# Kernel tuning notes

Measured on AMD Instinct MI355X. Metric: run time of the kernel, lower is better.

## Reference

```python
import jax, jax.numpy as jnp
import numpy as np

L = 4          # num_layers
D = 64         # embedding_dim
N = 100000     # nodes
E = 1250000    # edges
B = 2048       # graphs (batch.max()+1, fixed for jit)
ATOM_V = 128   # atom feature vocab per field
BOND_V = 8     # bond feature vocab per field
BN_EPS = 1e-5


def setup_inputs() -> dict:
    key = jax.random.key(0)
    ks = jax.random.split(key, 10)
    x_feat = jax.random.randint(ks[0], (N, 9), 0, 119)
    edge_index = jax.random.randint(ks[1], (2, E), 0, N)
    edge_attr = jax.random.randint(ks[2], (E, 3), 0, 5)
    batch = jnp.sort(jax.random.randint(ks[3], (N,), 0, B))
    s = 0.02
    atom_emb = jax.random.normal(ks[4], (9, ATOM_V, D), jnp.float32) * s
    bond_emb = jax.random.normal(ks[5], (L, 3, BOND_V, D), jnp.float32) * s
    eps = jnp.zeros((L,), jnp.float32)
    W1 = jax.random.normal(ks[6], (L, D, 2 * D), jnp.float32) / np.sqrt(D).astype(np.float32)
    b1 = jnp.zeros((L, 2 * D), jnp.float32)
    bn1_g = jnp.ones((L, 2 * D), jnp.float32)
    bn1_b = jnp.zeros((L, 2 * D), jnp.float32)
    W2 = jax.random.normal(ks[7], (L, 2 * D, D), jnp.float32) / np.sqrt(2 * D).astype(np.float32)
    b2 = jnp.zeros((L, D), jnp.float32)
    bn2_g = jnp.ones((L, D), jnp.float32)
    bn2_b = jnp.zeros((L, D), jnp.float32)
    return dict(atom_emb=atom_emb, bond_emb=bond_emb, eps=eps,
                W1=W1, b1=b1, bn1_g=bn1_g, bn1_b=bn1_b,
                W2=W2, b2=b2, bn2_g=bn2_g, bn2_b=bn2_b,
                x_feat=x_feat, edge_index=edge_index, edge_attr=edge_attr, batch=batch)


def _bn(h, g, b):
    # training-mode BatchNorm1d over node dim (biased variance, as torch forward)
    m = h.mean(axis=0)
    v = jnp.mean((h - m) ** 2, axis=0)
    return (h - m) * jax.lax.rsqrt(v + BN_EPS) * g + b


def reference(atom_emb, bond_emb, eps, W1, b1, bn1_g, bn1_b, W2, b2, bn2_g, bn2_b,
              x_feat, edge_index, edge_attr, batch):
    n = x_feat.shape[0]
    # AtomEncoder: sum of per-field embedding lookups -> [N, D]
    h = atom_emb[jnp.arange(9), x_feat].sum(axis=1)
    src, dst = edge_index[0], edge_index[1]
    for l in range(L):
        # BondEncoder for this layer: [E, D]
        e = bond_emb[l][jnp.arange(3), edge_attr].sum(axis=1)
        # message: relu(x_j + edge_emb); aggregate: scatter_add at target nodes
        msg = jax.nn.relu(h[src] + e)
        agg = jax.ops.segment_sum(msg, dst, num_segments=N)
        z = (1.0 + eps[l]) * h + agg
        # MLP: Linear -> BN -> ReLU -> Linear
        z = jax.nn.relu(_bn(z @ W1[l] + b1[l], bn1_g[l], bn1_b[l]))
        z = z @ W2[l] + b2[l]
        # outer per-layer BatchNorm
        h = _bn(z, bn2_g[l], bn2_b[l])
        if l != L - 1:
            h = jax.nn.relu(h)
        # dropout disabled (eval/deterministic reference)
    node_repr = h
    # mean pooling by graph id
    out_feat = jax.ops.segment_sum(h, batch, num_segments=B)
    cnt = jax.ops.segment_sum(jnp.ones((n, 1), h.dtype), batch, num_segments=B)
    graph_repr = out_feat / (cnt + 1e-9)
    return node_repr, graph_repr
```

## Files before the change

### kernel.cpp

```cpp
#include <hip/hip_runtime.h>

#define NN 100000
#define NE 1250000
#define NB 2048
#define NZB 391
#define NBK 196
#define BCAP 7168
#define ARND 2048

typedef __attribute__((ext_vector_type(8))) short short8;
typedef __attribute__((ext_vector_type(4))) float floatx4;

__device__ inline unsigned short f2bf(float f) {
    unsigned u = __float_as_uint(f);
    u = u + 0x7fffu + ((u >> 16) & 1u);
    return (unsigned short)(u >> 16);
}
__device__ inline float bf2f(unsigned short h) {
    return __uint_as_float(((unsigned)h) << 16);
}

__global__ void atom_encode(const float* __restrict__ atom_emb,
                            const int* __restrict__ x_feat,
                            float* __restrict__ h, unsigned short* __restrict__ h16) {
    int id = blockIdx.x * 256 + threadIdx.x;
    int n = id >> 4, q = id & 15;
    floatx4 acc = {0.f, 0.f, 0.f, 0.f};
    for (int f = 0; f < 9; f++) {
        int v = x_feat[n * 9 + f];
        const floatx4* p = (const floatx4*)(atom_emb + (size_t)(f * 128 + v) * 64);
        acc += p[q];
    }
    ((floatx4*)h)[(size_t)n * 16 + q] = acc;
    ushort4 hv;
    hv.x = f2bf(acc[0]); hv.y = f2bf(acc[1]); hv.z = f2bf(acc[2]); hv.w = f2bf(acc[3]);
    ((ushort4*)h16)[(size_t)n * 16 + q] = hv;
}


__launch_bounds__(256)
__global__ void bucketA(const int* __restrict__ ei, const int* __restrict__ ea,
                        int* __restrict__ bcnt, unsigned long long* __restrict__ bbuf) {
    __shared__ int cnt[256], inc[256], cur[256], gpos[256];
    __shared__ unsigned long long buf[ARND];
    __shared__ unsigned short bos[ARND];
    int tid = threadIdx.x;
    cnt[tid] = 0; cur[tid] = 0;
    __syncthreads();
    int base = blockIdx.x * ARND;
    unsigned long long rec[8]; int bb[8];
    #pragma unroll
    for (int i = 0; i < 8; i++) {
        int e = base + i * 256 + tid;
        if (e < NE) {
            int src = ei[e];
            int dst = ei[NE + e];
            unsigned at = (unsigned)(ea[e * 3] | (ea[e * 3 + 1] << 3) | (ea[e * 3 + 2] << 6));
            rec[i] = ((unsigned long long)(unsigned)dst << 32)
                   | (unsigned)src | (at << 17);
            bb[i] = dst >> 9;
            atomicAdd(&cnt[bb[i]], 1);
        } else bb[i] = -1;
    }
    __syncthreads();
    int v = cnt[tid];
    inc[tid] = v;
    __syncthreads();
    for (int d = 1; d < 256; d <<= 1) {
        int t = (tid >= d) ? inc[tid - d] : 0;
        __syncthreads();
        inc[tid] += t;
        __syncthreads();
    }
    if (v > 0) gpos[tid] = atomicAdd(&bcnt[tid], v);
    __syncthreads();
    #pragma unroll
    for (int i = 0; i < 8; i++) {
        if (bb[i] >= 0) {
            int b = bb[i];
            int p = atomicAdd(&cur[b], 1);
            int slot = (inc[b] - cnt[b]) + p;
            buf[slot] = rec[i];
            bos[slot] = (unsigned short)b;
        }
    }
    __syncthreads();
    int nval = inc[255];
    for (int s = tid; s < nval; s += 256) {
        int b = bos[s];
        int off = s - (inc[b] - cnt[b]);
        bbuf[(size_t)b * BCAP + gpos[b] + off] = buf[s];
    }
}

__launch_bounds__(256)
__global__ void bucketB(const int* __restrict__ bcnt,
                        const unsigned long long* __restrict__ bbuf,
                        int* __restrict__ csr, unsigned* __restrict__ epack) {
    __shared__ int c[512], cs[512], s[256], bp[256], sh[1];
    __shared__ unsigned long long fl[BCAP];
    int tid = threadIdx.x;
    int b = blockIdx.x;
    bp[tid] = (tid < NBK) ? bcnt[tid] : 0;
    c[tid] = 0; c[256 + tid] = 0;
    __syncthreads();
    for (int d = 1; d < 256; d <<= 1) {
        int t = (tid >= d) ? bp[tid - d] : 0;
        __syncthreads();
        bp[tid] += t;
        __syncthreads();
    }
    int gbase = b ? bp[b - 1] : 0;
    int cnt = bcnt[b];
    const unsigned long long* f = bbuf + (size_t)b * BCAP;
    int n0 = b << 9;
    for (int i = tid; i < cnt; i += 256) {
        unsigned long long v = f[i];
        fl[i] = v;
        atomicAdd(&c[(int)(v >> 32) - n0], 1);
    }
    __syncthreads();
    cs[tid] = c[tid]; cs[256 + tid] = c[256 + tid];
    s[tid] = c[tid];
    __syncthreads();
    for (int d = 1; d < 256; d <<= 1) {
        int t = (tid >= d) ? s[tid - d] : 0;
        __syncthreads();
        s[tid] += t;
        __syncthreads();
    }
    c[tid] = s[tid];
    if (tid == 255) sh[0] = s[255];
    __syncthreads();
    s[tid] = c[256 + tid];
    __syncthreads();
    for (int d = 1; d < 256; d <<= 1) {
        int t = (tid >= d) ? s[tid - d] : 0;
        __syncthreads();
        s[tid] += t;
        __syncthreads();
    }
    c[256 + tid] = s[tid] + sh[0];
    __syncthreads();
    int nn = NN - n0; if (nn > 512) nn = 512;
    for (int i = tid; i < 512; i += 256) {
        int start = gbase + c[i] - cs[i];
        if (i < nn) csr[n0 + i] = gbase + c[i];
        cs[i] = start;
    }
    __syncthreads();
    for (int t = 0; t < 8; t++) {
        for (int i = tid; i < cnt; i += 256) {
            unsigned long long v = fl[i];
            if ((int)((v & 0x1FFFFu) >> 14) == t) {
                int idx = (int)(v >> 32) - n0;
                int p = atomicAdd(&cs[idx], 1);
                epack[p] = (unsigned)v;
            }
        }
        __syncthreads();
    }
}

#define PROC(hh, rr, A)                                                       \
    {                                                                         \
        floatx4 m = {bf2f(hh.x), bf2f(hh.y), bf2f(hh.z), bf2f(hh.w)};         \
        if (HASBN) {                                                          \
            m[0] = fmaxf(cav[0] * m[0] + cbv[0], 0.f);                        \
            m[1] = fmaxf(cav[1] * m[1] + cbv[1], 0.f);                        \
            m[2] = fmaxf(cav[2] * m[2] + cbv[2], 0.f);                        \
            m[3] = fmaxf(cav[3] * m[3] + cbv[3], 0.f);                        \
        }                                                                     \
        m += beq[((rr >> 17) & 7u) * 16 + q];                                 \
        m += beq[(8 + ((rr >> 20) & 7u)) * 16 + q];                           \
        m += beq[(16 + ((rr >> 23) & 7u)) * 16 + q];                          \
        A[0] += fmaxf(m[0], 0.f);                                             \
        A[1] += fmaxf(m[1], 0.f);                                             \
        A[2] += fmaxf(m[2], 0.f);                                             \
        A[3] += fmaxf(m[3], 0.f);                                             \
    }

template <bool HASBN>
__global__ void gather_k(const float* __restrict__ x, const unsigned short* __restrict__ x16,
                         const float* __restrict__ bond_emb,
                         const float* __restrict__ eps, const int* __restrict__ csr,
                         const unsigned* __restrict__ epack, int l,
                         const float* __restrict__ stats, const float* __restrict__ bn_g,
                         const float* __restrict__ bn_b, float* __restrict__ agg) {
    __shared__ float be[24 * 64];
    __shared__ float ca[64], cb[64];
    int tid = threadIdx.x;
    const float* bsrc = bond_emb + (size_t)l * 1536;
    for (int i = tid; i < 1536; i += 256) be[i] = bsrc[i];
    if (tid < 64) {
        if (HASBN) {
            float s = 0.f, ss = 0.f;
            for (int j = 0; j < 8; j++) {
                s  += stats[j * 128 + tid];
                ss += stats[j * 128 + 64 + tid];
            }
            float mean = s / NN;
            float var  = ss / NN - mean * mean;
            float a = bn_g[(l - 1) * 64 + tid] * rsqrtf(var + 1e-5f);
            ca[tid] = a;
            cb[tid] = bn_b[(l - 1) * 64 + tid] - mean * a;
        } else {
            ca[tid] = 1.f; cb[tid] = 0.f;
        }
    }
    __syncthreads();
    int id = blockIdx.x * 256 + tid;
    int n = id >> 4, q = id & 15;
    float s = 1.0f + eps[l];
    floatx4 cav = *(const floatx4*)&ca[q * 4];
    floatx4 cbv = *(const floatx4*)&cb[q * 4];
    floatx4 xv = ((const floatx4*)x)[(size_t)n * 16 + q];
    if (HASBN) {
        xv[0] = fmaxf(cav[0] * xv[0] + cbv[0], 0.f);
        xv[1] = fmaxf(cav[1] * xv[1] + cbv[1], 0.f);
        xv[2] = fmaxf(cav[2] * xv[2] + cbv[2], 0.f);
        xv[3] = fmaxf(cav[3] * xv[3] + cbv[3], 0.f);
    }
    floatx4 acc = xv * s;
    floatx4 accB = {0.f, 0.f, 0.f, 0.f};
    int k0 = n ? csr[n - 1] : 0;
    int k1 = csr[n];
    const floatx4* beq = (const floatx4*)be;
    const ushort4* xq = (const ushort4*)x16;
    int k = k0;
    for (; k + 3 < k1; k += 4) {
        unsigned r0 = epack[k];
        unsigned r1 = epack[k + 1];
        unsigned r2 = epack[k + 2];
        unsigned r3 = epack[k + 3];
        ushort4 h0 = xq[(size_t)(r0 & 0x1FFFFu) * 16 + q];
        ushort4 h1 = xq[(size_t)(r1 & 0x1FFFFu) * 16 + q];
        ushort4 h2 = xq[(size_t)(r2 & 0x1FFFFu) * 16 + q];
        ushort4 h3 = xq[(size_t)(r3 & 0x1FFFFu) * 16 + q];
        __builtin_amdgcn_sched_barrier(0);
        PROC(h0, r0, acc)
        PROC(h1, r1, accB)
        PROC(h2, r2, acc)
        PROC(h3, r3, accB)
    }
    for (; k < k1; k++) {
        unsigned r0 = epack[k];
        ushort4 h0 = xq[(size_t)(r0 & 0x1FFFFu) * 16 + q];
        PROC(h0, r0, acc)
    }
    acc += accB;
    ((floatx4*)agg)[(size_t)n * 16 + q] = acc;
}

__global__ void wcvt(const float* __restrict__ W1, const float* __restrict__ W2,
                     unsigned short* __restrict__ w1h, unsigned short* __restrict__ w2h) {
    int id = blockIdx.x * 256 + threadIdx.x;
    if (id < 32768) {
        int l = id >> 13, rem = id & 8191, c = rem >> 6, k = rem & 63;
        w1h[id] = f2bf(W1[l * 8192 + k * 128 + c]);
    } else {
        int id2 = id - 32768;
        int l = id2 >> 13, rem = id2 & 8191, c = rem >> 7, k = rem & 127;
        w2h[id2] = f2bf(W2[l * 8192 + k * 64 + c]);
    }
}

#define MFMA __builtin_amdgcn_mfma_f32_16x16x32_bf16

#define ZS 264
__launch_bounds__(256)
__global__ void zstat(const float* __restrict__ z, float* __restrict__ G,
                      float* __restrict__ zsum) {
    __shared__ char smem[67584];
    unsigned short* zh = (unsigned short*)smem;
    unsigned short* zl = zh + 64 * ZS;
    int tid = threadIdx.x;
    int c2 = tid & 31;
    int nof = tid >> 5;
    int wv = tid >> 6, lane = tid & 63, m = lane & 15, qd = lane >> 4;
    float2 csum = make_float2(0.f, 0.f);
    floatx4 acc[8];
    for (int t = 0; t < 8; t++) acc[t] = (floatx4){0.f, 0.f, 0.f, 0.f};
    int base = blockIdx.x * 256;
    for (int it = 0; it < 32; it++) {
        int n = it * 8 + nof;
        int node = base + n;
        float2 v = make_float2(0.f, 0.f);
        if (node < NN) v = ((const float2*)z)[(size_t)node * 32 + c2];
        csum.x += v.x; csum.y += v.y;
        unsigned short hx = f2bf(v.x), hy = f2bf(v.y);
        zh[(2 * c2) * ZS + n] = hx;
        zh[(2 * c2 + 1) * ZS + n] = hy;
        zl[(2 * c2) * ZS + n] = f2bf(v.x - bf2f(hx));
        zl[(2 * c2 + 1) * ZS + n] = f2bf(v.y - bf2f(hy));
    }
    __syncthreads();
    for (int kc = 0; kc < 8; kc++) {
        short8 ah = *(const short8*)&zh[(wv * 16 + m) * ZS + kc * 32 + qd * 8];
        for (int j = 0; j < 4; j++) {
            short8 bh = *(const short8*)&zh[(j * 16 + m) * ZS + kc * 32 + qd * 8];
            short8 bl = *(const short8*)&zl[(j * 16 + m) * ZS + kc * 32 + qd * 8];
            acc[j * 2]     = MFMA(ah, bh, acc[j * 2], 0, 0, 0);
            acc[j * 2 + 1] = MFMA(ah, bl, acc[j * 2 + 1], 0, 0, 0);
        }
    }
    for (int j = 0; j < 4; j++)
        for (int r = 0; r < 4; r++) {
            int idx = (wv * 16 + qd * 4 + r) * 64 + j * 16 + m;
            atomicAdd(&G[idx], acc[j * 2][r]);
            atomicAdd(&G[4096 + idx], acc[j * 2 + 1][r]);
        }
    __syncthreads();
    float* red = (float*)smem;
    red[tid] = csum.x; red[256 + tid] = csum.y;
    __syncthreads();
    if (tid < 32) {
        float sx = 0.f, sy = 0.f;
        for (int k = 0; k < 8; k++) { sx += red[k * 32 + tid]; sy += red[256 + k * 32 + tid]; }
        atomicAdd(&zsum[2 * tid], sx);
        atomicAdd(&zsum[2 * tid + 1], sy);
    }
}

__launch_bounds__(256)
__global__ void bn1stat(const float* __restrict__ W1, const float* __restrict__ b1,
                        const float* __restrict__ G, const float* __restrict__ zsum,
                        int l, const float* __restrict__ bn_g, const float* __restrict__ bn_b,
                        float* __restrict__ cab) {
    __shared__ float wc[64];
    __shared__ float red[256];
    int c = blockIdx.x;
    int tid = threadIdx.x;
    if (tid < 64) wc[tid] = bf2f(f2bf(W1[l * 8192 + tid * 128 + c]));
    __syncthreads();
    float q = 0.f;
    for (int p = 0; p < 16; p++) {
        int idx = p * 256 + tid;
        int i = idx >> 6, j = idx & 63;
        q += wc[i] * wc[j] * (G[idx] + 2.f * G[4096 + idx]);
    }
    red[tid] = q;
    __syncthreads();
    for (int d = 128; d > 0; d >>= 1) {
        if (tid < d) red[tid] += red[tid + d];
        __syncthreads();
    }
    if (tid == 0) {
        float s1 = 0.f;
        for (int k = 0; k < 64; k++) s1 += zsum[k] * wc[k];
        float bc = b1[l * 128 + c];
        double mean = ((double)s1 + (double)NN * (double)bc) / (double)NN;
        double ex2  = ((double)red[0] + 2.0 * (double)bc * (double)s1
                       + (double)NN * (double)bc * (double)bc) / (double)NN;
        float var = (float)(ex2 - mean * mean);
        float a = bn_g[l * 128 + c] * rsqrtf(var + 1e-5f);
        cab[c] = a;
        cab[128 + c] = bn_b[l * 128 + c] - (float)mean * a + a * bc;
    }
}

#define RS 140
__launch_bounds__(256, 4)
__global__ void mlp_fused(const float* __restrict__ z,
                          const unsigned short* __restrict__ w1h,
                          const unsigned short* __restrict__ w2h,
                          const float* __restrict__ b2,
                          const float* __restrict__ cab, int l,
                          float* __restrict__ t2, unsigned short* __restrict__ t216,
                          float* __restrict__ s2f) {
    __shared__ unsigned short smem[4 * 2 * 16 * RS];
    int tid = threadIdx.x;
    int wv = tid >> 6, lane = tid & 63, m = lane & 15, qd = lane >> 4;
    int base = blockIdx.x * 64;
    unsigned short* rbh = smem + wv * (2 * 16 * RS);
    unsigned short* rbl = rbh + 16 * RS;

    int row = base + wv * 16 + m;
    floatx4 z0a = {0.f, 0.f, 0.f, 0.f}, z0b = z0a, z1a = z0a, z1b = z0a;
    if (row < NN) {
        const floatx4* zp = (const floatx4*)z + (size_t)row * 16;
        z0a = zp[qd * 2];
        z0b = zp[qd * 2 + 1];
        z1a = zp[8 + qd * 2];
        z1b = zp[8 + qd * 2 + 1];
    }
    short8 ah0, al0, ah1, al1;
    for (int j = 0; j < 4; j++) {
        unsigned short h;
        h = f2bf(z0a[j]); ah0[j] = (short)h; al0[j] = (short)f2bf(z0a[j] - bf2f(h));
        h = f2bf(z0b[j]); ah0[4 + j] = (short)h; al0[4 + j] = (short)f2bf(z0b[j] - bf2f(h));
        h = f2bf(z1a[j]); ah1[j] = (short)h; al1[j] = (short)f2bf(z1a[j] - bf2f(h));
        h = f2bf(z1b[j]); ah1[4 + j] = (short)h; al1[4 + j] = (short)f2bf(z1b[j] - bf2f(h));
    }

    float caT[8], cbT[8];
    #pragma unroll
    for (int t = 0; t < 8; t++) {
        caT[t] = cab[t * 16 + m];
        cbT[t] = cab[128 + t * 16 + m];
    }

    const unsigned short* w1p = w1h + l * 8192;
    floatx4 acc1[8];
    #pragma unroll
    for (int t = 0; t < 8; t++) {
        const unsigned short* wp = w1p + (t * 16 + m) * 64;
        short8 bh0 = *(const short8*)(wp + qd * 8);
        short8 bh1 = *(const short8*)(wp + 32 + qd * 8);
        floatx4 c0 = {0.f, 0.f, 0.f, 0.f};
        c0 = MFMA(ah0, bh0, c0, 0, 0, 0);
        c0 = MFMA(al0, bh0, c0, 0, 0, 0);
        c0 = MFMA(ah1, bh1, c0, 0, 0, 0);
        c0 = MFMA(al1, bh1, c0, 0, 0, 0);
        acc1[t] = c0;
    }

    #pragma unroll
    for (int t = 0; t < 8; t++) {
        float a = caT[t], b = cbT[t];
        #pragma unroll
        for (int r = 0; r < 4; r++) {
            int rl = qd * 4 + r;
            float rv = fmaxf(a * acc1[t][r] + b, 0.f);
            unsigned short hh = f2bf(rv);
            rbh[rl * RS + t * 16 + m] = hh;
            rbl[rl * RS + t * 16 + m] = f2bf(rv - bf2f(hh));
        }
    }
    short8 ahf[4], alf[4];
    #pragma unroll
    for (int kh = 0; kh < 4; kh++) {
        ahf[kh] = *(const short8*)&rbh[m * RS + kh * 32 + qd * 8];
        alf[kh] = *(const short8*)&rbl[m * RS + kh * 32 + qd * 8];
    }

    const unsigned short* w2p = w2h + l * 8192;
    floatx4 acc2[4];
    #pragma unroll
    for (int t = 0; t < 4; t++) {
        const unsigned short* wp = w2p + (t * 16 + m) * 128;
        floatx4 c0 = {0.f, 0.f, 0.f, 0.f};
        #pragma unroll
        for (int kh = 0; kh < 4; kh++) {
            short8 bh = *(const short8*)(wp + kh * 32 + qd * 8);
            c0 = MFMA(ahf[kh], bh, c0, 0, 0, 0);
            c0 = MFMA(alf[kh], bh, c0, 0, 0, 0);
        }
        acc2[t] = c0;
    }

    float* redw = (float*)rbh;
    const float* bias = b2 + l * 64;
    #pragma unroll
    for (int t = 0; t < 4; t++) {
        int col = t * 16 + m;
        float bv = bias[col];
        float s = 0.f, ss = 0.f;
        #pragma unroll
        for (int r = 0; r < 4; r++) {
            int node = base + wv * 16 + qd * 4 + r;
            if (node < NN) {
                float v = acc2[t][r] + bv;
                t2[(size_t)node * 64 + col] = v;
                t216[(size_t)node * 64 + col] = f2bf(v);
                s += v; ss += v * v;
            }
        }
        redw[col * 4 + qd] = s;
        redw[256 + col * 4 + qd] = ss;
    }
    __syncthreads();
    if (tid < 64) {
        float s = 0.f, ss = 0.f;
        for (int w = 0; w < 4; w++) {
            const float* rw = (const float*)(smem + w * (2 * 16 * RS));
            for (int q = 0; q < 4; q++) {
                s  += rw[tid * 4 + q];
                ss += rw[256 + tid * 4 + q];
            }
        }
        float* dst = s2f + (blockIdx.x & 7) * 128;
        atomicAdd(&dst[tid], s);
        atomicAdd(&dst[64 + tid], ss);
    }
}

__global__ void bnapply_last(const float* __restrict__ t2, const float* __restrict__ bn_g,
                             const float* __restrict__ bn_b, const float* __restrict__ s2f,
                             float* __restrict__ out, float* __restrict__ gsum,
                             float* __restrict__ gcnt, const int* __restrict__ batch) {
    __shared__ float ca[64], cb[64];
    int tid = threadIdx.x;
    if (tid < 64) {
        float s = 0.f, ss = 0.f;
        for (int j = 0; j < 8; j++) {
            s  += s2f[j * 128 + tid];
            ss += s2f[j * 128 + 64 + tid];
        }
        float mean = s / NN;
        float var  = ss / NN - mean * mean;
        float a = bn_g[3 * 64 + tid] * rsqrtf(var + 1e-5f);
        ca[tid] = a;
        cb[tid] = bn_b[3 * 64 + tid] - mean * a;
    }
    __syncthreads();
    int c = tid & 63, nsub = tid >> 6;
    int nodebase = blockIdx.x * 64;
    float accv = 0.f, accc = 0.f;
    int curg = -1;
    for (int it = 0; it < 16; it++) {
        int node = nodebase + it * 4 + nsub;
        if (node < NN) {
            float v = ca[c] * t2[(size_t)node * 64 + c] + cb[c];
            out[(size_t)node * 64 + c] = v;
            int g = batch[node];
            if (g != curg) {
                if (curg >= 0) {
                    atomicAdd(&gsum[(size_t)curg * 64 + c], accv);
                    if (c == 0) atomicAdd(&gcnt[curg], accc);
                }
                curg = g; accv = v; accc = 1.f;
            } else {
                accv += v; accc += 1.f;
            }
        }
    }
    if (curg >= 0) {
        atomicAdd(&gsum[(size_t)curg * 64 + c], accv);
        if (c == 0) atomicAdd(&gcnt[curg], accc);
    }
}

__global__ void pool_div(const float* __restrict__ gsum, const float* __restrict__ gcnt,
                         float* __restrict__ out) {
    int id = blockIdx.x * 256 + threadIdx.x;
    int g = id >> 6;
    out[(size_t)NN * 64 + id] = gsum[id] / (gcnt[g] + 1e-9f);
}

extern "C" void kernel_launch(void* const* d_in, const int* in_sizes, int n_in,
                              void* d_out, int out_size, void* d_ws, size_t ws_size,
                              hipStream_t stream) {
    const float* atom_emb = (const float*)d_in[0];
    const float* bond_emb = (const float*)d_in[1];
    const float* eps      = (const float*)d_in[2];
    const float* W1       = (const float*)d_in[3];
    const float* b1       = (const float*)d_in[4];
    const float* bn1_g    = (const float*)d_in[5];
    const float* bn1_b    = (const float*)d_in[6];
    const float* W2       = (const float*)d_in[7];
    const float* b2       = (const float*)d_in[8];
    const float* bn2_g    = (const float*)d_in[9];
    const float* bn2_b    = (const float*)d_in[10];
    const int* x_feat     = (const int*)d_in[11];
    const int* edge_index = (const int*)d_in[12];
    const int* edge_attr  = (const int*)d_in[13];
    const int* batch      = (const int*)d_in[14];
    float* out = (float*)d_out;

    char* ws = (char*)d_ws;
    float* gsum   = (float*)ws;   ws += (size_t)NB * 64 * 4;
    float* gcnt   = (float*)ws;   ws += NB * 4;
    float* zsum   = (float*)ws;   ws += 4 * 64 * 4;
    float* G      = (float*)ws;   ws += (size_t)4 * 8192 * 4;
    float* s2f    = (float*)ws;   ws += (size_t)4 * 8 * 128 * 4;
    int* bcnt     = (int*)ws;     ws += 256 * 4;
    size_t zbytes = (size_t)(ws - (char*)d_ws);
    int* csr        = (int*)ws;       ws += (size_t)NN * 4;
    float* cab      = (float*)ws;     ws += 256 * 4;
    unsigned* epack = (unsigned*)ws;  ws += (size_t)NE * 4;
    float* xbuf = (float*)ws;     ws += (size_t)NN * 64 * 4;
    unsigned short* x16 = (unsigned short*)ws; ws += (size_t)NN * 64 * 2;
    float* agg  = (float*)ws;     ws += (size_t)NN * 64 * 4;
    unsigned short* w1h = (unsigned short*)ws; ws += 32768 * 2;
    unsigned short* w2h = (unsigned short*)ws; ws += 32768 * 2;
    unsigned long long* bbuf = (unsigned long long*)ws; ws += (size_t)NBK * BCAP * 8;

    hipMemsetAsync((void*)gsum, 0, zbytes, stream);

    wcvt<<<256, 256, 0, stream>>>(W1, W2, w1h, w2h);
    bucketA<<<(NE + ARND - 1) / ARND, 256, 0, stream>>>(edge_index, edge_attr, bcnt, bbuf);
    bucketB<<<NBK, 256, 0, stream>>>(bcnt, bbuf, csr, epack);
    atom_encode<<<6250, 256, 0, stream>>>(atom_emb, x_feat, xbuf, x16);

    for (int l = 0; l < 4; l++) {
        if (l == 0) {
            gather_k<false><<<6250, 256, 0, stream>>>(xbuf, x16, bond_emb, eps, csr, epack, l,
                                                      nullptr, nullptr, nullptr, agg);
        } else {
            gather_k<true><<<6250, 256, 0, stream>>>(xbuf, x16, bond_emb, eps, csr, epack, l,
                                                     s2f + (size_t)(l - 1) * 1024,
                                                     bn2_g, bn2_b, agg);
        }
        float* Gl = G + (size_t)l * 8192;
        zstat<<<NZB, 256, 0, stream>>>(agg, Gl, zsum + l * 64);
        bn1stat<<<128, 256, 0, stream>>>(W1, b1, Gl, zsum + l * 64, l, bn1_g, bn1_b, cab);
        mlp_fused<<<1563, 256, 0, stream>>>(agg, w1h, w2h, b2, cab, l,
                                            xbuf, x16, s2f + (size_t)l * 1024);
    }
    bnapply_last<<<1563, 256, 0, stream>>>(xbuf, bn2_g, bn2_b, s2f + (size_t)3 * 1024,
                                           out, gsum, gcnt, batch);
    pool_div<<<512, 256, 0, stream>>>(gsum, gcnt, out);
}
```

Baseline: 740.2 us.

## Merge prep kernels into one launch and fold BN1 stats into zstat last block

```diff
diff --git a/kernel.cpp b/kernel.cpp
--- a/kernel.cpp
+++ b/kernel.cpp
@@ -7,6 +7,7 @@
 #define NBK 196
 #define BCAP 7168
 #define ARND 2048
+#define NAB 611
 
 typedef __attribute__((ext_vector_type(8))) short short8;
 typedef __attribute__((ext_vector_type(4))) float floatx4;
@@ -20,76 +21,88 @@
     return __uint_as_float(((unsigned)h) << 16);
 }
 
-__global__ void atom_encode(const float* __restrict__ atom_emb,
-                            const int* __restrict__ x_feat,
-                            float* __restrict__ h, unsigned short* __restrict__ h16) {
-    int id = blockIdx.x * 256 + threadIdx.x;
-    int n = id >> 4, q = id & 15;
-    floatx4 acc = {0.f, 0.f, 0.f, 0.f};
-    for (int f = 0; f < 9; f++) {
-        int v = x_feat[n * 9 + f];
-        const floatx4* p = (const floatx4*)(atom_emb + (size_t)(f * 128 + v) * 64);
-        acc += p[q];
-    }
-    ((floatx4*)h)[(size_t)n * 16 + q] = acc;
-    ushort4 hv;
-    hv.x = f2bf(acc[0]); hv.y = f2bf(acc[1]); hv.z = f2bf(acc[2]); hv.w = f2bf(acc[3]);
-    ((ushort4*)h16)[(size_t)n * 16 + q] = hv;
-}
-
-
 __launch_bounds__(256)
-__global__ void bucketA(const int* __restrict__ ei, const int* __restrict__ ea,
-                        int* __restrict__ bcnt, unsigned long long* __restrict__ bbuf) {
+__global__ void prep(const int* __restrict__ ei, const int* __restrict__ ea,
+                     int* __restrict__ bcnt, unsigned long long* __restrict__ bbuf,
+                     const float* __restrict__ atom_emb, const int* __restrict__ x_feat,
+                     float* __restrict__ h, unsigned short* __restrict__ h16,
+                     const float* __restrict__ W1, const float* __restrict__ W2,
+                     unsigned short* __restrict__ w1h, unsigned short* __restrict__ w2h) {
     __shared__ int cnt[256], inc[256], cur[256], gpos[256];
     __shared__ unsigned long long buf[ARND];
     __shared__ unsigned short bos[ARND];
     int tid = threadIdx.x;
-    cnt[tid] = 0; cur[tid] = 0;
-    __syncthreads();
-    int base = blockIdx.x * ARND;
-    unsigned long long rec[8]; int bb[8];
-    #pragma unroll
-    for (int i = 0; i < 8; i++) {
-        int e = base + i * 256 + tid;
-        if (e < NE) {
-            int src = ei[e];
-            int dst = ei[NE + e];
-            unsigned at = (unsigned)(ea[e * 3] | (ea[e * 3 + 1] << 3) | (ea[e * 3 + 2] << 6));
-            rec[i] = ((unsigned long long)(unsigned)dst << 32)
-                   | (unsigned)src | (at << 17);
-            bb[i] = dst >> 9;
-            atomicAdd(&cnt[bb[i]], 1);
-        } else bb[i] = -1;
-    }
-    __syncthreads();
-    int v = cnt[tid];
-    inc[tid] = v;
-    __syncthreads();
-    for (int d = 1; d < 256; d <<= 1) {
-        int t = (tid >= d) ? inc[tid - d] : 0;
-        __syncthreads();
-        inc[tid] += t;
-        __syncthreads();
-    }
-    if (v > 0) gpos[tid] = atomicAdd(&bcnt[tid], v);
-    __syncthreads();
-    #pragma unroll
-    for (int i = 0; i < 8; i++) {
-        if (bb[i] >= 0) {
-            int b = bb[i];
-            int p = atomicAdd(&cur[b], 1);
-            int slot = (inc[b] - cnt[b]) + p;
-            buf[slot] = rec[i];
-            bos[slot] = (unsigned short)b;
-        }
-    }
-    __syncthreads();
-    int nval = inc[255];
-    for (int s = tid; s < nval; s += 256) {
-        int b = bos[s];
-        int off = s - (inc[b] - cnt[b]);
-        bbuf[(size_t)b * BCAP + gpos[b] + off] = buf[s];
+    int bid = blockIdx.x;
+    if (bid < NAB) {
+        cnt[tid] = 0; cur[tid] = 0;
+        __syncthreads();
+        int base = bid * ARND;
+        unsigned long long rec[8]; int bb[8];
+        #pragma unroll
+        for (int i = 0; i < 8; i++) {
+            int e = base + i * 256 + tid;
+            if (e < NE) {
+                int src = ei[e];
+                int dst = ei[NE + e];
+                unsigned at = (unsigned)(ea[e * 3] | (ea[e * 3 + 1] << 3) | (ea[e * 3 + 2] << 6));
+                rec[i] = ((unsigned long long)(unsigned)dst << 32)
+                       | (unsigned)src | (at << 17);
+                bb[i] = dst >> 9;
+                atomicAdd(&cnt[bb[i]], 1);
+            } else bb[i] = -1;
+        }
+        __syncthreads();
+        int v = cnt[tid];
+        inc[tid] = v;
+        __syncthreads();
+        for (int d = 1; d < 256; d <<= 1) {
+            int t = (tid >= d) ? inc[tid - d] : 0;
+            __syncthreads();
+            inc[tid] += t;
+            __syncthreads();
+        }
+        if (v > 0) gpos[tid] = atomicAdd(&bcnt[tid], v);
+        __syncthreads();
+        #pragma unroll
+        for (int i = 0; i < 8; i++) {
+            if (bb[i] >= 0) {
+                int b = bb[i];
+                int p = atomicAdd(&cur[b], 1);
+                int slot = (inc[b] - cnt[b]) + p;
+                buf[slot] = rec[i];
+                bos[slot] = (unsigned short)b;
+            }
+        }
+        __syncthreads();
+        int nval = inc[255];
+        for (int s = tid; s < nval; s += 256) {
+            int b = bos[s];
+            int off = s - (inc[b] - cnt[b]);
+            bbuf[(size_t)b * BCAP + gpos[b] + off] = buf[s];
+        }
+    } else if (bid < NAB + 6250) {
+        int id = (bid - NAB) * 256 + tid;
+        int n = id >> 4, q = id & 15;
+        floatx4 acc = {0.f, 0.f, 0.f, 0.f};
+        for (int f = 0; f < 9; f++) {
+            int vv = x_feat[n * 9 + f];
+            const floatx4* p = (const floatx4*)(atom_emb + (size_t)(f * 128 + vv) * 64);
+            acc += p[q];
+        }
+        ((floatx4*)h)[(size_t)n * 16 + q] = acc;
+        ushort4 hv;
+        hv.x = f2bf(acc[0]); hv.y = f2bf(acc[1]); hv.z = f2bf(acc[2]); hv.w = f2bf(acc[3]);
+        ((ushort4*)h16)[(size_t)n * 16 + q] = hv;
+    } else {
+        int id = (bid - NAB - 6250) * 256 + tid;
+        if (id < 32768) {
+            int l = id >> 13, rem = id & 8191, c = rem >> 6, k = rem & 63;
+            w1h[id] = f2bf(W1[l * 8192 + k * 128 + c]);
+        } else {
+            int id2 = id - 32768;
+            int l = id2 >> 13, rem = id2 & 8191, c = rem >> 7, k = rem & 127;
+            w2h[id2] = f2bf(W2[l * 8192 + k * 64 + c]);
+        }
     }
 }
 
@@ -252,25 +265,15 @@
     ((floatx4*)agg)[(size_t)n * 16 + q] = acc;
 }
 
-__global__ void wcvt(const float* __restrict__ W1, const float* __restrict__ W2,
-                     unsigned short* __restrict__ w1h, unsigned short* __restrict__ w2h) {
-    int id = blockIdx.x * 256 + threadIdx.x;
-    if (id < 32768) {
-        int l = id >> 13, rem = id & 8191, c = rem >> 6, k = rem & 63;
-        w1h[id] = f2bf(W1[l * 8192 + k * 128 + c]);
-    } else {
-        int id2 = id - 32768;
-        int l = id2 >> 13, rem = id2 & 8191, c = rem >> 7, k = rem & 127;
-        w2h[id2] = f2bf(W2[l * 8192 + k * 64 + c]);
-    }
-}
-
 #define MFMA __builtin_amdgcn_mfma_f32_16x16x32_bf16
 
 #define ZS 264
 __launch_bounds__(256)
 __global__ void zstat(const float* __restrict__ z, float* __restrict__ G,
-                      float* __restrict__ zsum) {
+                      float* __restrict__ zsum,
+                      const float* __restrict__ W1, const float* __restrict__ b1,
+                      const float* __restrict__ bn_g, const float* __restrict__ bn_b,
+                      float* __restrict__ cab, int* __restrict__ zcnt, int l) {
     __shared__ char smem[67584];
     unsigned short* zh = (unsigned short*)smem;
     unsigned short* zl = zh + 64 * ZS;
@@ -320,37 +323,35 @@
         atomicAdd(&zsum[2 * tid], sx);
         atomicAdd(&zsum[2 * tid + 1], sy);
     }
-}
-
-__launch_bounds__(256)
-__global__ void bn1stat(const float* __restrict__ W1, const float* __restrict__ b1,
-                        const float* __restrict__ G, const float* __restrict__ zsum,
-                        int l, const float* __restrict__ bn_g, const float* __restrict__ bn_b,
-                        float* __restrict__ cab) {
-    __shared__ float wc[64];
-    __shared__ float red[256];
-    int c = blockIdx.x;
-    int tid = threadIdx.x;
-    if (tid < 64) wc[tid] = bf2f(f2bf(W1[l * 8192 + tid * 128 + c]));
-    __syncthreads();
-    float q = 0.f;
-    for (int p = 0; p < 16; p++) {
-        int idx = p * 256 + tid;
-        int i = idx >> 6, j = idx & 63;
-        q += wc[i] * wc[j] * (G[idx] + 2.f * G[4096 + idx]);
-    }
-    red[tid] = q;
-    __syncthreads();
-    for (int d = 128; d > 0; d >>= 1) {
-        if (tid < d) red[tid] += red[tid + d];
-        __syncthreads();
-    }
-    if (tid == 0) {
+    __threadfence();
+    int* flag = (int*)(smem + 2048);
+    if (tid == 0) flag[0] = atomicAdd(zcnt, 1);
+    __syncthreads();
+    if (flag[0] != NZB - 1) return;
+    __threadfence();
+    float* wcs = (float*)(smem + 4096);
+    const float* W1p = W1 + l * 8192;
+    for (int i2 = tid; i2 < 8192; i2 += 256) wcs[i2] = bf2f(f2bf(W1p[i2]));
+    __syncthreads();
+    int c = tid >> 1, hh = tid & 1;
+    const volatile float* Gv = G;
+    float qq = 0.f;
+    for (int i = hh * 32; i < hh * 32 + 32; i++) {
+        float wi = wcs[i * 128 + c];
+        for (int j = 0; j < 64; j++) {
+            float g0 = Gv[i * 64 + j];
+            float g1 = Gv[4096 + i * 64 + j];
+            qq += wi * wcs[j * 128 + c] * (g0 + 2.f * g1);
+        }
+    }
+    qq += __shfl_xor(qq, 1);
+    if (hh == 0) {
+        const volatile float* zs = zsum;
         float s1 = 0.f;
-        for (int k = 0; k < 64; k++) s1 += zsum[k] * wc[k];
+        for (int kk = 0; kk < 64; kk++) s1 += zs[kk] * wcs[kk * 128 + c];
         float bc = b1[l * 128 + c];
         double mean = ((double)s1 + (double)NN * (double)bc) / (double)NN;
-        double ex2  = ((double)red[0] + 2.0 * (double)bc * (double)s1
+        double ex2  = ((double)qq + 2.0 * (double)bc * (double)s1
                        + (double)NN * (double)bc * (double)bc) / (double)NN;
         float var = (float)(ex2 - mean * mean);
         float a = bn_g[l * 128 + c] * rsqrtf(var + 1e-5f);
@@ -565,6 +566,7 @@
     float* G      = (float*)ws;   ws += (size_t)4 * 8192 * 4;
     float* s2f    = (float*)ws;   ws += (size_t)4 * 8 * 128 * 4;
     int* bcnt     = (int*)ws;     ws += 256 * 4;
+    int* zcnt     = (int*)ws;     ws += 16;
     size_t zbytes = (size_t)(ws - (char*)d_ws);
     int* csr        = (int*)ws;       ws += (size_t)NN * 4;
     float* cab      = (float*)ws;     ws += 256 * 4;
@@ -578,10 +580,10 @@
 
     hipMemsetAsync((void*)gsum, 0, zbytes, stream);
 
-    wcvt<<<256, 256, 0, stream>>>(W1, W2, w1h, w2h);
-    bucketA<<<(NE + ARND - 1) / ARND, 256, 0, stream>>>(edge_index, edge_attr, bcnt, bbuf);
+    prep<<<NAB + 6250 + 256, 256, 0, stream>>>(edge_index, edge_attr, bcnt, bbuf,
+                                               atom_emb, x_feat, xbuf, x16,
+                                               W1, W2, w1h, w2h);
     bucketB<<<NBK, 256, 0, stream>>>(bcnt, bbuf, csr, epack);
-    atom_encode<<<6250, 256, 0, stream>>>(atom_emb, x_feat, xbuf, x16);
 
     for (int l = 0; l < 4; l++) {
         if (l == 0) {
@@ -593,8 +595,8 @@
                                                      bn2_g, bn2_b, agg);
         }
         float* Gl = G + (size_t)l * 8192;
-        zstat<<<NZB, 256, 0, stream>>>(agg, Gl, zsum + l * 64);
-        bn1stat<<<128, 256, 0, stream>>>(W1, b1, Gl, zsum + l * 64, l, bn1_g, bn1_b, cab);
+        zstat<<<NZB, 256, 0, stream>>>(agg, Gl, zsum + l * 64,
+                                       W1, b1, bn1_g, bn1_b, cab, zcnt + l, l);
         mlp_fused<<<1563, 256, 0, stream>>>(agg, w1h, w2h, b2, cab, l,
                                             xbuf, x16, s2f + (size_t)l * 1024);
     }
```

Result: slower. 2.315 ms (+212.8%).
